# Kernel tuning notes

Measured on AMD Instinct MI355X. Metric: run time of the kernel, lower is better.

Reference implementation:

```python
import jax, jax.numpy as jnp
import numpy as np


def _pairwise_sqdist(a, b):
    # a: [B,N,3], b: [B,M,3] -> [B,N,M] squared L2 distances
    a2 = jnp.sum(a * a, axis=-1)            # [B,N]
    b2 = jnp.sum(b * b, axis=-1)            # [B,M]
    ab = jnp.einsum('bnd,bmd->bnm', a, b)   # [B,N,M]
    d = a2[:, :, None] + b2[:, None, :] - 2.0 * ab
    return jnp.maximum(d, 0.0)


def setup_inputs() -> dict:
    key = jax.random.key(0)
    k1, k2 = jax.random.split(key)
    B, N, M = 4, 8192, 8192
    p1 = jax.random.normal(k1, (B, N, 3), dtype=jnp.float32)
    p2 = jax.random.normal(k2, (B, M, 3), dtype=jnp.float32)
    return {"p1": p1, "p2": p2}


def reference(p1, p2):
    # chamfer_3DDist: squared L2 NN distances both directions, then mean of each
    d = _pairwise_sqdist(p1, p2)   # [B,N,M]
    d1 = jnp.min(d, axis=2)        # [B,N] nearest p2 for each p1 point
    d2 = jnp.min(d, axis=1)        # [B,M] nearest p1 for each p2 point
    return jnp.mean(d1) + jnp.mean(d2)
```

## Files before the change

kernel.cpp:

```cpp
#include <hip/hip_runtime.h>
#include <float.h>


typedef short sh8    __attribute__((ext_vector_type(8)));
typedef float f32x16 __attribute__((ext_vector_type(16)));

#define BLK   256
#define BATCH 4
#define NPTS  8192
#define PCH   8
#define PCHUNK (NPTS / PCH)
#define QA    2
#define QPW   (QA * 32)
#define QPB   (4 * QPW)
#define QTILES (NPTS / QPB)
#define GRID  (2 * BATCH * QTILES * PCH)
#define TOTQ  (2 * BATCH * NPTS)
#define WS_NEED ((size_t)PCH * TOTQ * sizeof(float))
#define ONEBF 0x3F80

__device__ __forceinline__ short f2bf(float f) {
    unsigned u = __float_as_uint(f);
    unsigned r = (u + 0x7FFFu + ((u >> 16) & 1u)) >> 16;
    return (short)r;
}
__device__ __forceinline__ float bf2f(short h) {
    return __uint_as_float(((unsigned)(unsigned short)h) << 16);
}

__global__ void zero_out_kernel(float* out) { out[0] = 0.f; }

__global__ __launch_bounds__(BLK, 2) void cd_mfma_kernel(
    const float* __restrict__ p1, const float* __restrict__ p2,
    float* __restrict__ part)
{
    __shared__ uint4 ptsB[2 * PCHUNK];

    int bid    = blockIdx.x;
    int pchunk = bid & (PCH - 1);
    int qt     = (bid >> 3) & (QTILES - 1);
    int batch  = (bid >> 8) & (BATCH - 1);
    int dir    = bid >> 10;

    const float* qbase = (dir == 0 ? p1 : p2) + (size_t)batch * NPTS * 3;
    const float* dbase = (dir == 0 ? p2 : p1) + (size_t)batch * NPTS * 3;

    int tid  = threadIdx.x;
    int wave = tid >> 6;
    int lane = tid & 63;
    int col  = lane & 31;
    int half = lane >> 5;

    #pragma unroll
    for (int it = 0; it < PCHUNK / BLK; ++it) {
        int p = tid + it * BLK;
        const float* s = dbase + (size_t)(pchunk * PCHUNK + p) * 3;
        float x = s[0], y = s[1], z = s[2];
        short hx = f2bf(x), hy = f2bf(y), hz = f2bf(z);
        short lx = f2bf(x - bf2f(hx));
        short ly = f2bf(y - bf2f(hy));
        short lz = f2bf(z - bf2f(hz));
        float w = -0.5f * (x * x + y * y + z * z);
        short wh = f2bf(w);
        short wl = f2bf(w - bf2f(wh));
        unsigned uhx = (unsigned short)hx, uhy = (unsigned short)hy, uhz = (unsigned short)hz;
        unsigned ulx = (unsigned short)lx, uly = (unsigned short)ly, ulz = (unsigned short)lz;
        ptsB[p] = make_uint4(uhx | (uhy << 16), uhz | (uhx << 16),
                             uhy | (uhz << 16), ulx | (uly << 16));
        ptsB[PCHUNK + p] = make_uint4(
            ulz | (ulx << 16), uly | (ulz << 16),
            (unsigned)(unsigned short)wh | ((unsigned)(unsigned short)wl << 16),
            ((unsigned)ONEBF) | (((unsigned)ONEBF) << 16));
    }

    sh8 afrag[QA];
    #pragma unroll
    for (int qa = 0; qa < QA; ++qa) {
        int q = qt * QPB + wave * QPW + qa * 32 + col;
        const float* s = qbase + (size_t)q * 3;
        float x = s[0], y = s[1], z = s[2];
        short hx = f2bf(x), hy = f2bf(y), hz = f2bf(z);
        short lx = f2bf(x - bf2f(hx));
        short ly = f2bf(y - bf2f(hy));
        short lz = f2bf(z - bf2f(hz));
        float w = -0.5f * (x * x + y * y + z * z);
        short nh = f2bf(w);
        short nl = f2bf(w - bf2f(nh));
        afrag[qa][0] = half ? hz : hx;
        afrag[qa][1] = half ? lx : hy;
        afrag[qa][2] = half ? ly : hz;
        afrag[qa][3] = half ? lz : lx;
        afrag[qa][4] = half ? (short)ONEBF : ly;
        afrag[qa][5] = half ? (short)ONEBF : lz;
        afrag[qa][6] = half ? nh : hx;
        afrag[qa][7] = half ? nl : hy;
    }
    __syncthreads();

    f32x16 zc;
    f32x16 runmax[QA];
    #pragma unroll
    for (int i = 0; i < 16; ++i) zc[i] = 0.f;
    #pragma unroll
    for (int qa = 0; qa < QA; ++qa)
        #pragma unroll
        for (int i = 0; i < 16; ++i) runmax[qa][i] = -FLT_MAX;

    const uint4* bbase = ptsB + half * PCHUNK + col;

    #pragma unroll 2
    for (int t = 0; t < PCHUNK / 32; t += 2) {
        sh8 b0 = *(const sh8*)(bbase + t * 32);
        sh8 b1 = *(const sh8*)(bbase + (t + 1) * 32);
        #pragma unroll
        for (int qa = 0; qa < QA; ++qa) {
            f32x16 a0 = __builtin_amdgcn_mfma_f32_32x32x16_bf16(
                afrag[qa], b0, zc, 0, 0, 0);
            f32x16 a1 = __builtin_amdgcn_mfma_f32_32x32x16_bf16(
                afrag[qa], b1, zc, 0, 0, 0);
            runmax[qa] = __builtin_elementwise_max(
                runmax[qa], __builtin_elementwise_max(a0, a1));
        }
    }

    int qglob0 = dir * (BATCH * NPTS) + batch * NPTS + qt * QPB + wave * QPW;
    float* prow = part + (size_t)pchunk * TOTQ + qglob0;
    #pragma unroll
    for (int qa = 0; qa < QA; ++qa) {
        f32x16 rm = runmax[qa];
        #pragma unroll
        for (int step = 1; step <= 16; step <<= 1) {
            f32x16 o;
            #pragma unroll
            for (int i = 0; i < 16; ++i) o[i] = __shfl_xor(rm[i], step, 64);
            rm = __builtin_elementwise_max(rm, o);
        }
        if (col == 0) {
            #pragma unroll
            for (int reg = 0; reg < 16; ++reg) {
                int r = (reg & 3) + 8 * (reg >> 2) + 4 * half;
                prow[qa * 32 + r] = fmaxf(-2.f * rm[reg], 0.f);
            }
        }
    }
}

__global__ __launch_bounds__(BLK) void min_sum_kernel(
    const float* __restrict__ part, float* __restrict__ out, float scale)
{
    int qid = blockIdx.x * BLK + threadIdx.x;
    float v = FLT_MAX;
    #pragma unroll
    for (int m = 0; m < PCH; ++m)
        v = fminf(v, part[(size_t)m * TOTQ + qid]);
    for (int off = 32; off > 0; off >>= 1) v += __shfl_down(v, off, 64);
    __shared__ float wsum[BLK / 64];
    int lane = threadIdx.x & 63, wid = threadIdx.x >> 6;
    if (lane == 0) wsum[wid] = v;
    __syncthreads();
    if (threadIdx.x == 0) {
        float t = 0.f;
        for (int w = 0; w < BLK / 64; ++w) t += wsum[w];
        atomicAdd(out, t * scale);
    }
}

typedef float v2f __attribute__((ext_vector_type(2)));
typedef float v4f __attribute__((ext_vector_type(4)));
#define FQPT   8
#define FNCH   32
#define FCHUNK (NPTS / FNCH)

__global__ __launch_bounds__(BLK) void init_kernel(unsigned* mins, float* out, int n) {
    int i = blockIdx.x * BLK + threadIdx.x;
    if (i < n) mins[i] = 0x7F7FFFFFu;
    if (i == 0) out[0] = 0.f;
}

__global__ __launch_bounds__(BLK) void cd_chunk_atomic_kernel(
    const float* __restrict__ p1, const float* __restrict__ p2,
    unsigned* __restrict__ mins)
{
    __shared__ v4f pts[FCHUNK];
    int bid    = blockIdx.x;
    int mchunk = bid & (FNCH - 1);
    int qt     = (bid >> 5) & 3;
    int batch  = (bid >> 7) & (BATCH - 1);
    int dir    = bid >> 9;
    const float* qbase = (dir == 0 ? p1 : p2) + (size_t)batch * NPTS * 3;
    const float* dbase = (dir == 0 ? p2 : p1) + (size_t)batch * NPTS * 3;
    int tid = threadIdx.x;
    if (tid < FCHUNK / 4) {
        int t4 = tid * 4;
        const float* s = dbase + (size_t)(mchunk * FCHUNK + t4) * 3;
        float4 f0 = *(const float4*)(s);
        float4 f1 = *(const float4*)(s + 4);
        float4 f2 = *(const float4*)(s + 8);
        float x0 = f0.x, y0 = f0.y, z0 = f0.z;
        float x1 = f0.w, y1 = f1.x, z1 = f1.y;
        float x2 = f1.z, y2 = f1.w, z2 = f2.x;
        float x3 = f2.y, y3 = f2.z, z3 = f2.w;
        float w0 = -0.5f * (x0*x0 + y0*y0 + z0*z0);
        float w1 = -0.5f * (x1*x1 + y1*y1 + z1*z1);
        float w2 = -0.5f * (x2*x2 + y2*y2 + z2*z2);
        float w3 = -0.5f * (x3*x3 + y3*y3 + z3*z3);
        pts[4*tid + 0] = (v4f){x0, x1, y0, y1};
        pts[4*tid + 1] = (v4f){z0, z1, w0, w1};
        pts[4*tid + 2] = (v4f){x2, x3, y2, y3};
        pts[4*tid + 3] = (v4f){z2, z3, w2, w3};
    }
    v2f qx2[FQPT], qy2[FQPT], qz2[FQPT];
    float qn[FQPT];
    #pragma unroll
    for (int k = 0; k < FQPT; ++k) {
        int q = qt * (BLK * FQPT) + k * BLK + tid;
        const float* s = qbase + (size_t)q * 3;
        float qx = s[0], qy = s[1], qz = s[2];
        qx2[k] = (v2f){qx, qx}; qy2[k] = (v2f){qy, qy}; qz2[k] = (v2f){qz, qz};
        qn[k] = qx * qx + qy * qy + qz * qz;
    }
    __syncthreads();
    v2f acc0[FQPT], acc1[FQPT];
    #pragma unroll
    for (int k = 0; k < FQPT; ++k) {
        acc0[k] = (v2f){-FLT_MAX, -FLT_MAX};
        acc1[k] = (v2f){-FLT_MAX, -FLT_MAX};
    }
    #pragma unroll 2
    for (int m = 0; m < FCHUNK / 2; m += 2) {
        v4f u0 = pts[2*m + 0], v0 = pts[2*m + 1];
        v4f u1 = pts[2*m + 2], v1 = pts[2*m + 3];
        v2f X0 = __builtin_shufflevector(u0, u0, 0, 1);
        v2f Y0 = __builtin_shufflevector(u0, u0, 2, 3);
        v2f Z0 = __builtin_shufflevector(v0, v0, 0, 1);
        v2f W0 = __builtin_shufflevector(v0, v0, 2, 3);
        v2f X1 = __builtin_shufflevector(u1, u1, 0, 1);
        v2f Y1 = __builtin_shufflevector(u1, u1, 2, 3);
        v2f Z1 = __builtin_shufflevector(v1, v1, 0, 1);
        v2f W1 = __builtin_shufflevector(v1, v1, 2, 3);
        #pragma unroll
        for (int k = 0; k < FQPT; ++k) {
            v2f s0 = __builtin_elementwise_fma(qz2[k], Z0,
                      __builtin_elementwise_fma(qy2[k], Y0,
                       __builtin_elementwise_fma(qx2[k], X0, W0)));
            acc0[k] = __builtin_elementwise_max(acc0[k], s0);
            v2f s1 = __builtin_elementwise_fma(qz2[k], Z1,
                      __builtin_elementwise_fma(qy2[k], Y1,
                       __builtin_elementwise_fma(qx2[k], X1, W1)));
            acc1[k] = __builtin_elementwise_max(acc1[k], s1);
        }
    }
    unsigned qid = (unsigned)(dir * (BATCH * NPTS) + batch * NPTS + qt * (BLK * FQPT) + tid);
    #pragma unroll
    for (int k = 0; k < FQPT; ++k) {
        float mx = fmaxf(fmaxf(acc0[k].x, acc0[k].y), fmaxf(acc1[k].x, acc1[k].y));
        float d = fmaxf(qn[k] - 2.f * mx, 0.f);
        atomicMin(&mins[qid + k * BLK], __float_as_uint(d));
    }
}

__global__ __launch_bounds__(BLK) void sum_kernel(
    const unsigned* __restrict__ mins, float* __restrict__ out, int n, float scale)
{
    int i = blockIdx.x * BLK + threadIdx.x;
    int stride = gridDim.x * BLK;
    float v = 0.f;
    for (int idx = i; idx < n; idx += stride) v += __uint_as_float(mins[idx]);
    for (int off = 32; off > 0; off >>= 1) v += __shfl_down(v, off, 64);
    __shared__ float wsum[BLK / 64];
    int lane = threadIdx.x & 63, wid = threadIdx.x >> 6;
    if (lane == 0) wsum[wid] = v;
    __syncthreads();
    if (threadIdx.x == 0) {
        float t = 0.f;
        for (int w = 0; w < BLK / 64; ++w) t += wsum[w];
        atomicAdd(out, t * scale);
    }
}

extern "C" void kernel_launch(void* const* d_in, const int* in_sizes, int n_in,
                              void* d_out, int out_size, void* d_ws, size_t ws_size,
                              hipStream_t stream) {
    const float* p1 = (const float*)d_in[0];
    const float* p2 = (const float*)d_in[1];
    float* out = (float*)d_out;

    if (ws_size >= WS_NEED) {
        float* part = (float*)d_ws;
        zero_out_kernel<<<1, 1, 0, stream>>>(out);
        cd_mfma_kernel<<<GRID, BLK, 0, stream>>>(p1, p2, part);
        min_sum_kernel<<<TOTQ / BLK, BLK, 0, stream>>>(part, out,
                                                       1.f / (float)(BATCH * NPTS));
    } else {
        unsigned* mins = (unsigned*)d_ws;
        init_kernel<<<TOTQ / BLK, BLK, 0, stream>>>(mins, out, TOTQ);
        cd_chunk_atomic_kernel<<<1024, BLK, 0, stream>>>(p1, p2, mins);
        sum_kernel<<<64, BLK, 0, stream>>>(mins, out, TOTQ, 1.f / (float)(BATCH * NPTS));
    }
}
```

Measured before the change: 103.1 us.

## Compute both chamfer directions from one distance tile with column-min atomics

The kernel previously ran each direction separately, computing the full N×M dot-product matrix twice. Now each tile's MFMA results feed both the row maxima and per-column maxima, which are reduced across the wave and merged into a shared-memory column buffer with atomicMin on float bits. This halves the grid and the MFMA work. In exchange it adds extra max reductions, cross-lane shuffles and LDS atomics in the inner loop, a second partial-result buffer, and one more reduction launch.

Result: faster. 99.42 us (-3.6%).

```diff
diff --git a/kernel.cpp b/kernel.cpp
--- a/kernel.cpp
+++ b/kernel.cpp
@@ -14,10 +14,11 @@
 #define QPW   (QA * 32)
 #define QPB   (4 * QPW)
 #define QTILES (NPTS / QPB)
-#define GRID  (2 * BATCH * QTILES * PCH)
-#define TOTQ  (2 * BATCH * NPTS)
-#define WS_NEED ((size_t)PCH * TOTQ * sizeof(float))
+#define GRID  (BATCH * QTILES * PCH)
+#define NROW  (BATCH * NPTS)
+#define WS_NEED ((size_t)(PCH + QTILES) * NROW * sizeof(float))
 #define ONEBF 0x3F80
+#define NEGMAXU 0xFF7FFFFFu
 
 __device__ __forceinline__ short f2bf(float f) {
     unsigned u = __float_as_uint(f);
@@ -27,23 +28,33 @@
 __device__ __forceinline__ float bf2f(short h) {
     return __uint_as_float(((unsigned)(unsigned short)h) << 16);
 }
+__device__ __forceinline__ float tree_max16(f32x16 v) {
+    float a = fmaxf(fmaxf(v[0], v[1]), v[2]);
+    float b = fmaxf(fmaxf(v[3], v[4]), v[5]);
+    float c = fmaxf(fmaxf(v[6], v[7]), v[8]);
+    float d = fmaxf(fmaxf(v[9], v[10]), v[11]);
+    float e = fmaxf(fmaxf(v[12], v[13]), v[14]);
+    float f = fmaxf(fmaxf(a, b), c);
+    float g = fmaxf(fmaxf(d, e), v[15]);
+    return fmaxf(f, g);
+}
 
 __global__ void zero_out_kernel(float* out) { out[0] = 0.f; }
 
 __global__ __launch_bounds__(BLK, 2) void cd_mfma_kernel(
     const float* __restrict__ p1, const float* __restrict__ p2,
-    float* __restrict__ part)
+    float* __restrict__ part1, float* __restrict__ part2)
 {
     __shared__ uint4 ptsB[2 * PCHUNK];
+    __shared__ unsigned colbuf[PCHUNK];
 
     int bid    = blockIdx.x;
     int pchunk = bid & (PCH - 1);
     int qt     = (bid >> 3) & (QTILES - 1);
-    int batch  = (bid >> 8) & (BATCH - 1);
-    int dir    = bid >> 10;
-
-    const float* qbase = (dir == 0 ? p1 : p2) + (size_t)batch * NPTS * 3;
-    const float* dbase = (dir == 0 ? p2 : p1) + (size_t)batch * NPTS * 3;
+    int batch  = bid >> 8;
+
+    const float* qbase = p1 + (size_t)batch * NPTS * 3;
+    const float* dbase = p2 + (size_t)batch * NPTS * 3;
 
     int tid  = threadIdx.x;
     int wave = tid >> 6;
@@ -54,6 +65,7 @@
     #pragma unroll
     for (int it = 0; it < PCHUNK / BLK; ++it) {
         int p = tid + it * BLK;
+        colbuf[p] = NEGMAXU;
         const float* s = dbase + (size_t)(pchunk * PCHUNK + p) * 3;
         float x = s[0], y = s[1], z = s[2];
         short hx = f2bf(x), hy = f2bf(y), hz = f2bf(z);
@@ -112,19 +124,26 @@
     for (int t = 0; t < PCHUNK / 32; t += 2) {
         sh8 b0 = *(const sh8*)(bbase + t * 32);
         sh8 b1 = *(const sh8*)(bbase + (t + 1) * 32);
-        #pragma unroll
-        for (int qa = 0; qa < QA; ++qa) {
-            f32x16 a0 = __builtin_amdgcn_mfma_f32_32x32x16_bf16(
-                afrag[qa], b0, zc, 0, 0, 0);
-            f32x16 a1 = __builtin_amdgcn_mfma_f32_32x32x16_bf16(
-                afrag[qa], b1, zc, 0, 0, 0);
-            runmax[qa] = __builtin_elementwise_max(
-                runmax[qa], __builtin_elementwise_max(a0, a1));
-        }
-    }
-
-    int qglob0 = dir * (BATCH * NPTS) + batch * NPTS + qt * QPB + wave * QPW;
-    float* prow = part + (size_t)pchunk * TOTQ + qglob0;
+        f32x16 a00 = __builtin_amdgcn_mfma_f32_32x32x16_bf16(afrag[0], b0, zc, 0, 0, 0);
+        f32x16 a10 = __builtin_amdgcn_mfma_f32_32x32x16_bf16(afrag[1], b0, zc, 0, 0, 0);
+        f32x16 a01 = __builtin_amdgcn_mfma_f32_32x32x16_bf16(afrag[0], b1, zc, 0, 0, 0);
+        f32x16 a11 = __builtin_amdgcn_mfma_f32_32x32x16_bf16(afrag[1], b1, zc, 0, 0, 0);
+        runmax[0] = __builtin_elementwise_max(runmax[0],
+                     __builtin_elementwise_max(a00, a01));
+        runmax[1] = __builtin_elementwise_max(runmax[1],
+                     __builtin_elementwise_max(a10, a11));
+        f32x16 c0 = __builtin_elementwise_max(a00, a10);
+        f32x16 c1 = __builtin_elementwise_max(a01, a11);
+        float m0 = tree_max16(c0);
+        float m1 = tree_max16(c1);
+        m0 = fmaxf(m0, __shfl_xor(m0, 32, 64));
+        m1 = fmaxf(m1, __shfl_xor(m1, 32, 64));
+        atomicMin(&colbuf[t * 32 + col], __float_as_uint(m0));
+        atomicMin(&colbuf[(t + 1) * 32 + col], __float_as_uint(m1));
+    }
+
+    int row0 = batch * NPTS + qt * QPB + wave * QPW;
+    float* prow = part1 + (size_t)pchunk * NROW + row0;
     #pragma unroll
     for (int qa = 0; qa < QA; ++qa) {
         f32x16 rm = runmax[qa];
@@ -143,16 +162,25 @@
             }
         }
     }
+
+    __syncthreads();
+    float* pcol = part2 + (size_t)qt * NROW + batch * NPTS + pchunk * PCHUNK;
+    #pragma unroll
+    for (int it = 0; it < PCHUNK / BLK; ++it) {
+        int c = tid + it * BLK;
+        float s = __uint_as_float(colbuf[c]);
+        pcol[c] = fmaxf(-2.f * s, 0.f);
+    }
 }
 
 __global__ __launch_bounds__(BLK) void min_sum_kernel(
-    const float* __restrict__ part, float* __restrict__ out, float scale)
+    const float* __restrict__ part, float* __restrict__ out,
+    int nparts, float scale)
 {
     int qid = blockIdx.x * BLK + threadIdx.x;
     float v = FLT_MAX;
-    #pragma unroll
-    for (int m = 0; m < PCH; ++m)
-        v = fminf(v, part[(size_t)m * TOTQ + qid]);
+    for (int m = 0; m < nparts; ++m)
+        v = fminf(v, part[(size_t)m * NROW + qid]);
     for (int off = 32; off > 0; off >>= 1) v += __shfl_down(v, off, 64);
     __shared__ float wsum[BLK / 64];
     int lane = threadIdx.x & 63, wid = threadIdx.x >> 6;
@@ -170,6 +198,7 @@
 #define FQPT   8
 #define FNCH   32
 #define FCHUNK (NPTS / FNCH)
+#define TOTQ  (2 * BATCH * NPTS)
 
 __global__ __launch_bounds__(BLK) void init_kernel(unsigned* mins, float* out, int n) {
     int i = blockIdx.x * BLK + threadIdx.x;
@@ -286,11 +315,14 @@
     float* out = (float*)d_out;
 
     if (ws_size >= WS_NEED) {
-        float* part = (float*)d_ws;
+        float* part1 = (float*)d_ws;
+        float* part2 = part1 + (size_t)PCH * NROW;
         zero_out_kernel<<<1, 1, 0, stream>>>(out);
-        cd_mfma_kernel<<<GRID, BLK, 0, stream>>>(p1, p2, part);
-        min_sum_kernel<<<TOTQ / BLK, BLK, 0, stream>>>(part, out,
-                                                       1.f / (float)(BATCH * NPTS));
+        cd_mfma_kernel<<<GRID, BLK, 0, stream>>>(p1, p2, part1, part2);
+        min_sum_kernel<<<NROW / BLK, BLK, 0, stream>>>(part1, out, PCH,
+                                                       1.f / (float)NROW);
+        min_sum_kernel<<<NROW / BLK, BLK, 0, stream>>>(part2, out, QTILES,
+                                                       1.f / (float)NROW);
     } else {
         unsigned* mins = (unsigned*)d_ws;
         init_kernel<<<TOTQ / BLK, BLK, 0, stream>>>(mins, out, TOTQ);
```
